# Kernel tuning notes

Hardware: AMD Instinct MI355X
Metric: run time of the kernel (lower is better)

The kernel has to match this reference:

```python
import jax, jax.numpy as jnp
import numpy as np

B, N, N0, C, HID, HEADS, SR = 8, 4096, 16384, 64, 256, 1, 8
EPS = 1e-6


def layernorm(x, w, b):
    m = x.mean(-1, keepdims=True)
    v = ((x - m) ** 2).mean(-1, keepdims=True)
    return (x - m) / jnp.sqrt(v + 1e-5) * w + b


def pixel_index(loc_orig, H, W):
    # loc_orig in [-1,1] -> nearest pixel index in flattened HxW map
    loc = (jnp.clip(loc_orig, -1.0, 1.0) + 1.0) * 0.5
    xi = jnp.clip(jnp.round(loc[..., 0] * (W - 1)).astype(jnp.int32), 0, W - 1)
    yi = jnp.clip(jnp.round(loc[..., 1] * (H - 1)).astype(jnp.int32), 0, H - 1)
    return yi * W + xi  # [B, N0]


def token2map(tok, pix, idx_agg, H, W):
    # token2map_agg_sparse: scatter-mean token features onto HxW grid (NHWC)
    Bc, Nt, Cc = tok.shape
    val = jnp.take_along_axis(tok, idx_agg[..., None], axis=1)  # [B,N0,C]
    def scat(v, p):
        s = jnp.zeros((H * W, Cc), v.dtype).at[p].add(v)
        cnt = jnp.zeros((H * W,), v.dtype).at[p].add(jnp.ones((), v.dtype))
        return s / (cnt[:, None] + EPS)
    m = jax.vmap(scat)(val, pix)  # [B,HW,C]
    return m.reshape(Bc, H, W, Cc)


def map2token_nearest(fmap, Nt, pix, idx_agg, agg_weight):
    # map2token_agg_fast_nearest: nearest gather + per-token weighted average
    Bc, H, W, Cc = fmap.shape
    flat = fmap.reshape(Bc, H * W, Cc)
    val = jnp.take_along_axis(flat, pix[..., None], axis=1)  # [B,N0,C]
    def agg(v, w, idx):
        sw = jnp.zeros((Nt,), w.dtype).at[idx].add(w)
        nw = w / (sw[idx] + EPS)
        return jnp.zeros((Nt, Cc), v.dtype).at[idx].add(v * nw[:, None])
    return jax.vmap(agg)(val, agg_weight[..., 0], idx_agg)


def setup_inputs() -> dict:
    key = jax.random.key(0)
    ks = jax.random.split(key, 16)
    std = 0.02
    return dict(
        x=jax.random.normal(ks[0], (B, N, C), jnp.float32),
        loc_orig=jax.random.uniform(ks[1], (B, N0, 2), jnp.float32, -1.0, 1.0),
        idx_agg=jax.random.randint(ks[2], (B, N0), 0, N),
        agg_weight=jax.random.uniform(ks[3], (B, N0, 1), jnp.float32),
        H=128, W=128,
        n1_w=jnp.ones(C), n1_b=jnp.zeros(C),
        n2_w=jnp.ones(C), n2_b=jnp.zeros(C),
        q_w=jax.random.normal(ks[4], (C, C)) * std, q_b=jnp.zeros(C),
        kv_w=jax.random.normal(ks[5], (2 * C, C)) * std, kv_b=jnp.zeros(2 * C),
        proj_w=jax.random.normal(ks[6], (C, C)) * std, proj_b=jnp.zeros(C),
        sr_w=jax.random.normal(ks[7], (SR, SR, C, C)) * np.float32(np.sqrt(2.0 / (SR * SR * C))),
        sr_b=jnp.zeros(C), srn_w=jnp.ones(C), srn_b=jnp.zeros(C),
        fc1_w=jax.random.normal(ks[8], (HID, C)) * std, fc1_b=jnp.zeros(HID),
        dw_w=jax.random.normal(ks[9], (3, 3, 1, HID)) * np.float32(np.sqrt(2.0 / 9.0)),
        dw_b=jnp.zeros(HID),
        dwskip_w=jax.random.normal(ks[10], (HID,)) * std,
        fc2_w=jax.random.normal(ks[11], (C, HID)) * std, fc2_b=jnp.zeros(C),
    )


def reference(x, loc_orig, idx_agg, agg_weight, H, W,
              n1_w, n1_b, n2_w, n2_b, q_w, q_b, kv_w, kv_b, proj_w, proj_b,
              sr_w, sr_b, srn_w, srn_b, fc1_w, fc1_b, dw_w, dw_b, dwskip_w,
              fc2_w, fc2_b):
    Bc, Nt, Cc = x.shape
    hd = Cc // HEADS
    pix = pixel_index(loc_orig, H, W)

    # ---- attention (src_dict == input_dict, conf_source is None -> zeros) ----
    xn = layernorm(x, n1_w, n1_b)
    q = (xn @ q_w.T + q_b).reshape(Bc, Nt, HEADS, hd).transpose(0, 2, 1, 3)
    conf = jnp.zeros((Bc, Nt, 1), x.dtype)
    tmp = jnp.concatenate([xn, conf], -1)
    m = token2map(tmp, pix, idx_agg, H, W)            # [B,H,W,C+1]
    x_map, conf_map = m[..., :Cc], m[..., Cc:]
    xr = jax.lax.conv_general_dilated(x_map, sr_w, (SR, SR), 'VALID',
            dimension_numbers=('NHWC', 'HWIO', 'NHWC')) + sr_b
    h2, w2 = H // SR, W // SR
    xr = layernorm(xr.reshape(Bc, h2 * w2, Cc), srn_w, srn_b)
    conf_r = conf_map.reshape(Bc, h2, SR, w2, SR).mean((2, 4)).reshape(Bc, h2 * w2)
    kv = (xr @ kv_w.T + kv_b).reshape(Bc, h2 * w2, 2, HEADS, hd).transpose(2, 0, 3, 1, 4)
    k, v = kv[0], kv[1]
    attn = jnp.einsum('bhnd,bhmd->bhnm', q, k) * (hd ** -0.5) + conf_r[:, None, None, :]
    attn = jax.nn.softmax(attn, -1)
    ao = jnp.einsum('bhnm,bhmd->bhnd', attn, v).transpose(0, 2, 1, 3).reshape(Bc, Nt, Cc)
    x1 = x + (ao @ proj_w.T + proj_b)

    # ---- MLP with token2map -> depthwise conv -> map2token ----
    h = layernorm(x1, n2_w, n2_b) @ fc1_w.T + fc1_b   # [B,N,HID]
    hm = token2map(h, pix, idx_agg, H, W)             # [B,H,W,HID]
    hm = jax.lax.conv_general_dilated(hm, dw_w, (1, 1), 'SAME',
            dimension_numbers=('NHWC', 'HWIO', 'NHWC'),
            feature_group_count=HID) + dw_b
    h = map2token_nearest(hm, Nt, pix, idx_agg, agg_weight) + h * dwskip_w
    h = jax.nn.gelu(h, approximate=False)
    x2 = x1 + (h @ fc2_w.T + fc2_b)
    return x2
```

## Files before the change

### kernel.cpp

```cpp
#include <hip/hip_runtime.h>
#include <hip/hip_bf16.h>

#define DI __device__ __forceinline__


DI float wsum(float v){
#pragma unroll
  for (int o = 32; o; o >>= 1) v += __shfl_xor(v, o, 64);
  return v;
}
DI float wmax(float v){
#pragma unroll
  for (int o = 32; o; o >>= 1) v = fmaxf(v, __shfl_xor(v, o, 64));
  return v;
}
DI unsigned short f2b(float f){
  unsigned u = __float_as_uint(f);
  u = (u + 0x7FFFu + ((u >> 16) & 1u)) >> 16;
  return (unsigned short)u;
}
DI float b2f(unsigned short s){ return __uint_as_float(((unsigned)s) << 16); }

__global__ __launch_bounds__(256) void k_pix(const float* __restrict__ loc,
    const int* __restrict__ idx, const float* __restrict__ aw,
    int* __restrict__ pix, float* __restrict__ cnt, float* __restrict__ sw){
  int t = blockIdx.x * 256 + threadIdx.x;
  int b = t >> 14;
  float lx = (fminf(fmaxf(loc[2*t  ], -1.f), 1.f) + 1.f) * 0.5f;
  float ly = (fminf(fmaxf(loc[2*t+1], -1.f), 1.f) + 1.f) * 0.5f;
  int xi = (int)rintf(lx * 127.f); xi = min(max(xi, 0), 127);
  int yi = (int)rintf(ly * 127.f); yi = min(max(yi, 0), 127);
  int p = yi * 128 + xi;
  pix[t] = p;
  atomicAdd(&cnt[(b << 14) + p], 1.f);
  atomicAdd(&sw[(b << 12) + idx[t]], aw[t]);
}

__global__ __launch_bounds__(256) void k_lnq(const float* __restrict__ x,
    const float* __restrict__ n1w, const float* __restrict__ n1b,
    const float* __restrict__ qw, const float* __restrict__ qb,
    float* __restrict__ xn, float* __restrict__ q){
  __shared__ float wq[64*64];
  int tid = threadIdx.x;
  { int j = tid & 63, cp = tid >> 6;
    for (int cc = 0; cc < 16; ++cc){ int c = cp*16 + cc; wq[c*64 + j] = qw[j*64 + c]; } }
  __syncthreads();
  int lane = tid & 63, w = tid >> 6;
  for (int rr = 0; rr < 16; ++rr){
    int row = blockIdx.x * 64 + w * 16 + rr;
    float xv = x[row*64 + lane];
    float m = wsum(xv) * (1.f/64.f);
    float d = xv - m;
    float var = wsum(d*d) * (1.f/64.f);
    float xnv = d * rsqrtf(var + 1e-5f) * n1w[lane] + n1b[lane];
    xn[row*64 + lane] = xnv;
    float acc = qb[lane];
#pragma unroll
    for (int c = 0; c < 64; ++c) acc += __shfl(xnv, c, 64) * wq[c*64 + lane];
    q[row*64 + lane] = acc;
  }
}

__global__ __launch_bounds__(256) void k_scat1(const float* __restrict__ xn,
    const int* __restrict__ idx, const int* __restrict__ pix, float* __restrict__ s1){
  int t = blockIdx.x * 4 + (threadIdx.x >> 6);
  int lane = threadIdx.x & 63;
  int b = t >> 14;
  int j = idx[t], p = pix[t];
  atomicAdd(&s1[(((b << 14) + p) << 6) + lane], xn[(((b << 12) + j) << 6) + lane]);
}

__global__ __launch_bounds__(256) void k_srkv(const float* __restrict__ s1,
    const float* __restrict__ cnt, const float* __restrict__ srw, const float* __restrict__ srb,
    const float* __restrict__ snw, const float* __restrict__ snb,
    const float* __restrict__ kvw, const float* __restrict__ kvb,
    float* __restrict__ kb, float* __restrict__ vb){
  __shared__ unsigned short wl[256*64];
  __shared__ float patch[8*256];
  int tid = threadIdx.x;
  int oy = blockIdx.x >> 4, ox = blockIdx.x & 15;
  int oc = tid & 63, bg = tid >> 6;
  float acc0 = 0.f, acc1 = 0.f;
  for (int ch = 0; ch < 16; ++ch){
    for (int u = 0; u < 64; ++u){
      int e = u*256 + tid;
      wl[e] = f2b(srw[ch*16384 + e]);
    }
    for (int u = 0; u < 8; ++u){
      int e = u*256 + tid;
      int bb = e >> 8, r = e & 255;
      int pi = ch*4 + (r >> 6), ic = r & 63;
      int gp = (oy*8 + (pi >> 3))*128 + ox*8 + (pi & 7);
      int pidx = (bb << 14) + gp;
      patch[bb*256 + r] = s1[(pidx << 6) + ic] * (1.f/(cnt[pidx] + 1e-6f));
    }
    __syncthreads();
#pragma unroll 8
    for (int kk = 0; kk < 256; ++kk){
      float wv = b2f(wl[kk*64 + oc]);
      acc0 += patch[bg*256 + kk] * wv;
      acc1 += patch[(bg+4)*256 + kk] * wv;
    }
    __syncthreads();
  }
  int om = blockIdx.x;
  float t0 = acc0 + srb[oc];
  float t1 = acc1 + srb[oc];
  float m0 = wsum(t0) * (1.f/64.f), m1 = wsum(t1) * (1.f/64.f);
  float d0 = t0 - m0, d1 = t1 - m1;
  float v0 = wsum(d0*d0) * (1.f/64.f), v1 = wsum(d1*d1) * (1.f/64.f);
  float xr0 = d0 * rsqrtf(v0 + 1e-5f) * snw[oc] + snb[oc];
  float xr1 = d1 * rsqrtf(v1 + 1e-5f) * snw[oc] + snb[oc];
#pragma unroll
  for (int half = 0; half < 2; ++half){
    int j = half*64 + oc;
    float a0 = kvb[j], a1 = kvb[j];
#pragma unroll
    for (int c = 0; c < 64; ++c){
      float wv = kvw[j*64 + c];
      a0 += __shfl(xr0, c, 64) * wv;
      a1 += __shfl(xr1, c, 64) * wv;
    }
    float* dst = half ? vb : kb;
    dst[(((bg  )*256 + om) << 6) + oc] = a0;
    dst[(((bg+4)*256 + om) << 6) + oc] = a1;
  }
}

__global__ __launch_bounds__(256) void k_attn(const float* __restrict__ x,
    const float* __restrict__ q, const float* __restrict__ kb, const float* __restrict__ vb,
    const float* __restrict__ pw, const float* __restrict__ pb, float* __restrict__ x1){
  __shared__ unsigned short klp[16384];
  __shared__ unsigned short vlp[16384];
  int tid = threadIdx.x;
  int b = blockIdx.x >> 6;
  { int m = tid;
    for (int c = 0; c < 64; ++c){
      klp[c*256 + (m & 63)*4 + (m >> 6)] = f2b(kb[((b << 8) + m)*64 + c]);
      vlp[(m >> 2)*256 + c*4 + (m & 3)]  = f2b(vb[((b << 8) + m)*64 + c]);
    } }
  __syncthreads();
  int lane = tid & 63, w = tid >> 6;
  for (int rr = 0; rr < 16; ++rr){
    int row = blockIdx.x*64 + w*16 + rr;
    float qv = q[row*64 + lane];
    float sc0 = 0.f, sc1 = 0.f, sc2 = 0.f, sc3 = 0.f;
#pragma unroll
    for (int c = 0; c < 64; ++c){
      ushort4 k4 = *reinterpret_cast<const ushort4*>(&klp[c*256 + lane*4]);
      float qc = __shfl(qv, c, 64);
      sc0 += qc * b2f(k4.x); sc1 += qc * b2f(k4.y);
      sc2 += qc * b2f(k4.z); sc3 += qc * b2f(k4.w);
    }
    sc0 *= 0.125f; sc1 *= 0.125f; sc2 *= 0.125f; sc3 *= 0.125f;
    float mx = wmax(fmaxf(fmaxf(sc0, sc1), fmaxf(sc2, sc3)));
    float e[4];
    e[0] = __expf(sc0 - mx); e[1] = __expf(sc1 - mx);
    e[2] = __expf(sc2 - mx); e[3] = __expf(sc3 - mx);
    float r = 1.f / wsum(e[0] + e[1] + e[2] + e[3]);
    e[0] *= r; e[1] *= r; e[2] *= r; e[3] *= r;
    float acc = 0.f;
#pragma unroll
    for (int t = 0; t < 4; ++t){
#pragma unroll
      for (int gg = 0; gg < 16; ++gg){
        int g = t*16 + gg;
        ushort4 v4 = *reinterpret_cast<const ushort4*>(&vlp[(g*64 + lane)*4]);
        acc += __shfl(e[t], gg*4+0, 64) * b2f(v4.x)
             + __shfl(e[t], gg*4+1, 64) * b2f(v4.y)
             + __shfl(e[t], gg*4+2, 64) * b2f(v4.z)
             + __shfl(e[t], gg*4+3, 64) * b2f(v4.w);
      }
    }
    float pr = pb[lane];
#pragma unroll
    for (int c = 0; c < 64; ++c) pr += __shfl(acc, c, 64) * pw[lane*64 + c];
    x1[row*64 + lane] = x[row*64 + lane] + pr;
  }
}

__global__ __launch_bounds__(256) void k_lnfc1(const float* __restrict__ x1,
    const float* __restrict__ n2w, const float* __restrict__ n2b,
    const float* __restrict__ w1, const float* __restrict__ b1, float* __restrict__ h){
  __shared__ unsigned short wlp[16384];
  int tid = threadIdx.x;
  { int j = tid;
    for (int c = 0; c < 64; ++c)
      wlp[c*256 + (j & 63)*4 + (j >> 6)] = f2b(w1[j*64 + c]); }
  __syncthreads();
  int lane = tid & 63, w = tid >> 6;
  for (int rr = 0; rr < 16; ++rr){
    int row = blockIdx.x*64 + w*16 + rr;
    float xv = x1[row*64 + lane];
    float m = wsum(xv) * (1.f/64.f);
    float d = xv - m;
    float var = wsum(d*d) * (1.f/64.f);
    float xnv = d * rsqrtf(var + 1e-5f) * n2w[lane] + n2b[lane];
    float a0 = b1[lane], a1 = b1[64+lane], a2 = b1[128+lane], a3 = b1[192+lane];
#pragma unroll
    for (int c = 0; c < 64; ++c){
      ushort4 w4 = *reinterpret_cast<const ushort4*>(&wlp[c*256 + lane*4]);
      float xc = __shfl(xnv, c, 64);
      a0 += xc * b2f(w4.x); a1 += xc * b2f(w4.y);
      a2 += xc * b2f(w4.z); a3 += xc * b2f(w4.w);
    }
    int base = row*256 + lane;
    h[base] = a0; h[base+64] = a1; h[base+128] = a2; h[base+192] = a3;
  }
}

__global__ __launch_bounds__(256) void k_scat2(const float* __restrict__ h,
    const int* __restrict__ idx, const int* __restrict__ pix, float* __restrict__ hms){
  int t = blockIdx.x;
  int b = t >> 14;
  int j = idx[t], p = pix[t];
  int c = threadIdx.x;
  atomicAdd(&hms[((size_t)((b << 14) + p) << 8) + c], h[(((b << 12) + j) << 8) + c]);
}

__global__ __launch_bounds__(256) void k_dwgather(const float* __restrict__ hms,
    const float* __restrict__ cnt, const float* __restrict__ dww, const float* __restrict__ dwb,
    const int* __restrict__ idx, const int* __restrict__ pix,
    const float* __restrict__ aw, const float* __restrict__ sw, float* __restrict__ h2){
  int t = blockIdx.x;
  int b = t >> 14;
  int j = idx[t], p = pix[t];
  int y = p >> 7, xx = p & 127;
  int c = threadIdx.x;
  float a = dwb[c];
#pragma unroll
  for (int dy = -1; dy <= 1; ++dy){
    int yy = y + dy; if (yy < 0 || yy > 127) continue;
#pragma unroll
    for (int dx = -1; dx <= 1; ++dx){
      int xp = xx + dx; if (xp < 0 || xp > 127) continue;
      int pp = (b << 14) + yy*128 + xp;
      float ic = 1.f/(cnt[pp] + 1e-6f);
      a += hms[((size_t)pp << 8) + c] * ic * dww[((dy+1)*3 + dx+1)*256 + c];
    }
  }
  float nw = aw[t] / (sw[(b << 12) + j] + 1e-6f);
  atomicAdd(&h2[(((b << 12) + j) << 8) + c], a * nw);
}

__global__ __launch_bounds__(256) void k_fc2(const float* __restrict__ h2,
    const float* __restrict__ h, const float* __restrict__ dskip,
    const float* __restrict__ w2, const float* __restrict__ b2,
    const float* __restrict__ x1, float* __restrict__ out){
  __shared__ unsigned short wlp[16384];
  int tid = threadIdx.x;
  { int c = tid & 63, kp = tid >> 6;
    for (int kk = 0; kk < 64; ++kk){
      int k = kp*64 + kk;
      wlp[(k >> 2)*256 + c*4 + (k & 3)] = f2b(w2[c*256 + k]);
    } }
  __syncthreads();
  int lane = tid & 63, w = tid >> 6;
  for (int rr = 0; rr < 16; ++rr){
    int row = blockIdx.x*64 + w*16 + rr;
    int base = row*256 + lane;
    float g[4];
#pragma unroll
    for (int tt = 0; tt < 4; ++tt){
      float hv = h2[base + 64*tt] + h[base + 64*tt] * dskip[lane + 64*tt];
      g[tt] = 0.5f * hv * (1.f + erff(hv * 0.70710678118654752f));
    }
    float acc = b2[lane];
#pragma unroll
    for (int t = 0; t < 4; ++t){
#pragma unroll
      for (int gg = 0; gg < 16; ++gg){
        int kg = t*16 + gg;
        ushort4 w4 = *reinterpret_cast<const ushort4*>(&wlp[(kg*64 + lane)*4]);
        acc += __shfl(g[t], gg*4+0, 64) * b2f(w4.x)
             + __shfl(g[t], gg*4+1, 64) * b2f(w4.y)
             + __shfl(g[t], gg*4+2, 64) * b2f(w4.z)
             + __shfl(g[t], gg*4+3, 64) * b2f(w4.w);
      }
    }
    out[row*64 + lane] = x1[row*64 + lane] + acc;
  }
}

extern "C" void kernel_launch(void* const* d_in, const int* in_sizes, int n_in,
                              void* d_out, int out_size, void* d_ws, size_t ws_size,
                              hipStream_t stream){
  const float* x    = (const float*)d_in[0];
  const float* loc  = (const float*)d_in[1];
  const int*   idx  = (const int*)d_in[2];
  const float* aw   = (const float*)d_in[3];
  const float* n1w  = (const float*)d_in[6];
  const float* n1b  = (const float*)d_in[7];
  const float* n2w  = (const float*)d_in[8];
  const float* n2b  = (const float*)d_in[9];
  const float* qw   = (const float*)d_in[10];
  const float* qb   = (const float*)d_in[11];
  const float* kvw  = (const float*)d_in[12];
  const float* kvb  = (const float*)d_in[13];
  const float* pw   = (const float*)d_in[14];
  const float* pb   = (const float*)d_in[15];
  const float* srw  = (const float*)d_in[16];
  const float* srb  = (const float*)d_in[17];
  const float* snw  = (const float*)d_in[18];
  const float* snb  = (const float*)d_in[19];
  const float* w1   = (const float*)d_in[20];
  const float* b1   = (const float*)d_in[21];
  const float* dww  = (const float*)d_in[22];
  const float* dwb  = (const float*)d_in[23];
  const float* dskp = (const float*)d_in[24];
  const float* w2   = (const float*)d_in[25];
  const float* b2   = (const float*)d_in[26];
  float* out = (float*)d_out;

  float* ws = (float*)d_ws;
  int*   pix = (int*)ws;
  float* cnt = ws + 131072;
  float* sw  = ws + 262144;
  float* x1  = ws + 294912;
  float* h   = ws + 2392064;
  float* h2  = ws + 10780672;
  float* hms = ws + 19169280;
  float* s1  = hms;
  float* xn  = hms + 8388608;
  float* q   = hms + 10485760;
  float* kb  = hms + 12582912;
  float* vb  = hms + 12713984;

  hipMemsetAsync(cnt, 0, (size_t)(131072 + 32768) * 4, stream);
  hipMemsetAsync(s1,  0, (size_t)8388608 * 4, stream);
  hipMemsetAsync(h2,  0, (size_t)8388608 * 4, stream);

  k_pix   <<<512,    256, 0, stream>>>(loc, idx, aw, pix, cnt, sw);
  k_lnq   <<<512,    256, 0, stream>>>(x, n1w, n1b, qw, qb, xn, q);
  k_scat1 <<<32768,  256, 0, stream>>>(xn, idx, pix, s1);
  k_srkv  <<<256,    256, 0, stream>>>(s1, cnt, srw, srb, snw, snb, kvw, kvb, kb, vb);
  k_attn  <<<512,    256, 0, stream>>>(x, q, kb, vb, pw, pb, x1);
  k_lnfc1 <<<512,    256, 0, stream>>>(x1, n2w, n2b, w1, b1, h);

  hipMemsetAsync(hms, 0, (size_t)33554432 * 4, stream);

  k_scat2    <<<131072, 256, 0, stream>>>(h, idx, pix, hms);
  k_dwgather <<<131072, 256, 0, stream>>>(hms, cnt, dww, dwb, idx, pix, aw, sw, h2);
  k_fc2      <<<512,    256, 0, stream>>>(h2, h, dskp, w2, b2, x1, out);
}
```

Measured before the change: 1.422 ms.

## Pre-pack bf16 K/V in producer and read from global in attention kernel

The SR/KV kernel now writes K and V directly as bf16 in the packed layout attention expects, so the attention kernel no longer stages 64KB of converted K/V into LDS per block. Attention reads packed K/V from global/L2, processes two query rows per wave iteration, caches the transposed projection weight in LDS, and launches twice as many blocks with a 3-blocks/CU occupancy hint. This removes redundant per-block conversion and staging and raises occupancy, at the cost of repeated global/cache reads of K/V inside the inner loops.

Result: slower. 1.781 ms (+25.2%).

```diff
diff --git a/kernel.cpp b/kernel.cpp
--- a/kernel.cpp
+++ b/kernel.cpp
@@ -74,7 +74,7 @@
     const float* __restrict__ cnt, const float* __restrict__ srw, const float* __restrict__ srb,
     const float* __restrict__ snw, const float* __restrict__ snb,
     const float* __restrict__ kvw, const float* __restrict__ kvb,
-    float* __restrict__ kb, float* __restrict__ vb){
+    unsigned short* __restrict__ kpack, unsigned short* __restrict__ vpack){
   __shared__ unsigned short wl[256*64];
   __shared__ float patch[8*256];
   int tid = threadIdx.x;
@@ -121,61 +121,85 @@
       a0 += __shfl(xr0, c, 64) * wv;
       a1 += __shfl(xr1, c, 64) * wv;
     }
-    float* dst = half ? vb : kb;
-    dst[(((bg  )*256 + om) << 6) + oc] = a0;
-    dst[(((bg+4)*256 + om) << 6) + oc] = a1;
-  }
-}
-
-__global__ __launch_bounds__(256) void k_attn(const float* __restrict__ x,
-    const float* __restrict__ q, const float* __restrict__ kb, const float* __restrict__ vb,
+    if (half == 0){
+      int off = oc*256 + (om & 63)*4 + (om >> 6);
+      kpack[(bg    )*16384 + off] = f2b(a0);
+      kpack[(bg + 4)*16384 + off] = f2b(a1);
+    } else {
+      int off = (om >> 2)*256 + oc*4 + (om & 3);
+      vpack[(bg    )*16384 + off] = f2b(a0);
+      vpack[(bg + 4)*16384 + off] = f2b(a1);
+    }
+  }
+}
+
+__global__ __launch_bounds__(256, 3) void k_attn(const float* __restrict__ x,
+    const float* __restrict__ q, const unsigned short* __restrict__ kpack,
+    const unsigned short* __restrict__ vpack,
     const float* __restrict__ pw, const float* __restrict__ pb, float* __restrict__ x1){
-  __shared__ unsigned short klp[16384];
-  __shared__ unsigned short vlp[16384];
-  int tid = threadIdx.x;
-  int b = blockIdx.x >> 6;
-  { int m = tid;
+  __shared__ float pwl[64*64];
+  int tid = threadIdx.x;
+  for (int u = 0; u < 16; ++u){
+    int e = u*256 + tid;
+    pwl[e] = pw[(e & 63)*64 + (e >> 6)];
+  }
+  __syncthreads();
+  int bi = blockIdx.x;
+  int b  = bi >> 7;
+  int lane = tid & 63, w = tid >> 6;
+  const unsigned short* kp = kpack + b*16384;
+  const unsigned short* vp = vpack + b*16384;
+  float pbv = pb[lane];
+  for (int pi = 0; pi < 4; ++pi){
+    int row0 = (bi << 5) + (w << 3) + pi*2;
+    int row1 = row0 + 1;
+    float qv0 = q[row0*64 + lane], qv1 = q[row1*64 + lane];
+    float s0[4] = {0.f,0.f,0.f,0.f}, s1v[4] = {0.f,0.f,0.f,0.f};
+#pragma unroll
     for (int c = 0; c < 64; ++c){
-      klp[c*256 + (m & 63)*4 + (m >> 6)] = f2b(kb[((b << 8) + m)*64 + c]);
-      vlp[(m >> 2)*256 + c*4 + (m & 3)]  = f2b(vb[((b << 8) + m)*64 + c]);
-    } }
-  __syncthreads();
-  int lane = tid & 63, w = tid >> 6;
-  for (int rr = 0; rr < 16; ++rr){
-    int row = blockIdx.x*64 + w*16 + rr;
-    float qv = q[row*64 + lane];
-    float sc0 = 0.f, sc1 = 0.f, sc2 = 0.f, sc3 = 0.f;
-#pragma unroll
-    for (int c = 0; c < 64; ++c){
-      ushort4 k4 = *reinterpret_cast<const ushort4*>(&klp[c*256 + lane*4]);
-      float qc = __shfl(qv, c, 64);
-      sc0 += qc * b2f(k4.x); sc1 += qc * b2f(k4.y);
-      sc2 += qc * b2f(k4.z); sc3 += qc * b2f(k4.w);
-    }
-    sc0 *= 0.125f; sc1 *= 0.125f; sc2 *= 0.125f; sc3 *= 0.125f;
-    float mx = wmax(fmaxf(fmaxf(sc0, sc1), fmaxf(sc2, sc3)));
-    float e[4];
-    e[0] = __expf(sc0 - mx); e[1] = __expf(sc1 - mx);
-    e[2] = __expf(sc2 - mx); e[3] = __expf(sc3 - mx);
-    float r = 1.f / wsum(e[0] + e[1] + e[2] + e[3]);
-    e[0] *= r; e[1] *= r; e[2] *= r; e[3] *= r;
-    float acc = 0.f;
+      ushort4 k4 = *reinterpret_cast<const ushort4*>(kp + c*256 + lane*4);
+      float qc0 = __shfl(qv0, c, 64);
+      float qc1 = __shfl(qv1, c, 64);
+      float k0 = b2f(k4.x), k1 = b2f(k4.y), k2 = b2f(k4.z), k3 = b2f(k4.w);
+      s0[0] += qc0*k0; s0[1] += qc0*k1; s0[2] += qc0*k2; s0[3] += qc0*k3;
+      s1v[0] += qc1*k0; s1v[1] += qc1*k1; s1v[2] += qc1*k2; s1v[3] += qc1*k3;
+    }
+#pragma unroll
+    for (int t = 0; t < 4; ++t){ s0[t] *= 0.125f; s1v[t] *= 0.125f; }
+    float mx0 = wmax(fmaxf(fmaxf(s0[0], s0[1]), fmaxf(s0[2], s0[3])));
+    float mx1 = wmax(fmaxf(fmaxf(s1v[0], s1v[1]), fmaxf(s1v[2], s1v[3])));
+    float e0[4], e1[4];
+#pragma unroll
+    for (int t = 0; t < 4; ++t){ e0[t] = __expf(s0[t]-mx0); e1[t] = __expf(s1v[t]-mx1); }
+    float r0 = 1.f / wsum(e0[0]+e0[1]+e0[2]+e0[3]);
+    float r1 = 1.f / wsum(e1[0]+e1[1]+e1[2]+e1[3]);
+#pragma unroll
+    for (int t = 0; t < 4; ++t){ e0[t] *= r0; e1[t] *= r1; }
+    float a0 = 0.f, a1 = 0.f;
 #pragma unroll
     for (int t = 0; t < 4; ++t){
 #pragma unroll
       for (int gg = 0; gg < 16; ++gg){
         int g = t*16 + gg;
-        ushort4 v4 = *reinterpret_cast<const ushort4*>(&vlp[(g*64 + lane)*4]);
-        acc += __shfl(e[t], gg*4+0, 64) * b2f(v4.x)
-             + __shfl(e[t], gg*4+1, 64) * b2f(v4.y)
-             + __shfl(e[t], gg*4+2, 64) * b2f(v4.z)
-             + __shfl(e[t], gg*4+3, 64) * b2f(v4.w);
+        ushort4 v4 = *reinterpret_cast<const ushort4*>(vp + g*256 + lane*4);
+        float v0 = b2f(v4.x), v1 = b2f(v4.y), v2 = b2f(v4.z), v3 = b2f(v4.w);
+        float w0a = __shfl(e0[t], gg*4+0, 64), w0b = __shfl(e0[t], gg*4+1, 64);
+        float w0c = __shfl(e0[t], gg*4+2, 64), w0d = __shfl(e0[t], gg*4+3, 64);
+        float w1a = __shfl(e1[t], gg*4+0, 64), w1b = __shfl(e1[t], gg*4+1, 64);
+        float w1c = __shfl(e1[t], gg*4+2, 64), w1d = __shfl(e1[t], gg*4+3, 64);
+        a0 += w0a*v0 + w0b*v1 + w0c*v2 + w0d*v3;
+        a1 += w1a*v0 + w1b*v1 + w1c*v2 + w1d*v3;
       }
     }
-    float pr = pb[lane];
-#pragma unroll
-    for (int c = 0; c < 64; ++c) pr += __shfl(acc, c, 64) * pw[lane*64 + c];
-    x1[row*64 + lane] = x[row*64 + lane] + pr;
+    float pr0 = pbv, pr1 = pbv;
+#pragma unroll
+    for (int c = 0; c < 64; ++c){
+      float wv = pwl[c*64 + lane];
+      pr0 += __shfl(a0, c, 64) * wv;
+      pr1 += __shfl(a1, c, 64) * wv;
+    }
+    x1[row0*64 + lane] = x[row0*64 + lane] + pr0;
+    x1[row1*64 + lane] = x[row1*64 + lane] + pr1;
   }
 }
 
@@ -323,8 +347,8 @@
   float* s1  = hms;
   float* xn  = hms + 8388608;
   float* q   = hms + 10485760;
-  float* kb  = hms + 12582912;
-  float* vb  = hms + 12713984;
+  unsigned short* kpack = (unsigned short*)(hms + 12582912);
+  unsigned short* vpack = kpack + 131072;
 
   hipMemsetAsync(cnt, 0, (size_t)(131072 + 32768) * 4, stream);
   hipMemsetAsync(s1,  0, (size_t)8388608 * 4, stream);
@@ -333,8 +357,8 @@
   k_pix   <<<512,    256, 0, stream>>>(loc, idx, aw, pix, cnt, sw);
   k_lnq   <<<512,    256, 0, stream>>>(x, n1w, n1b, qw, qb, xn, q);
   k_scat1 <<<32768,  256, 0, stream>>>(xn, idx, pix, s1);
-  k_srkv  <<<256,    256, 0, stream>>>(s1, cnt, srw, srb, snw, snb, kvw, kvb, kb, vb);
-  k_attn  <<<512,    256, 0, stream>>>(x, q, kb, vb, pw, pb, x1);
+  k_srkv  <<<256,    256, 0, stream>>>(s1, cnt, srw, srb, snw, snb, kvw, kvb, kpack, vpack);
+  k_attn  <<<1024,   256, 0, stream>>>(x, q, kpack, vpack, pw, pb, x1);
   k_lnfc1 <<<512,    256, 0, stream>>>(x1, n2w, n2b, w1, b1, h);
 
   hipMemsetAsync(hms, 0, (size_t)33554432 * 4, stream);
```
